# Kernel optimization log

Hardware: AMD Instinct MI355X
Metric: run time of the kernel (lower is better)

Reference implementation:

```python
import jax, jax.numpy as jnp
import numpy as np

NU, NI, NA, D = 100000, 100000, 10000, 64
N0 = NU + NI        # user+item graph nodes
N1 = NU + NA        # user+author graph nodes
E0, E1, E3, E4, E5 = 6_400_000, 3_520_000, 1_000_000, 1_000_000, 2_000_000
N_LAYERS = 3
EPS = 1e-12


def setup_inputs() -> dict:
    key = jax.random.key(0)
    ks = jax.random.split(key, 18)
    inp = {
        'emb_user': 0.1 * jax.random.normal(ks[0], (NU, D), jnp.float32),
        'emb_item': 0.1 * jax.random.normal(ks[1], (NI, D), jnp.float32),
        'emb_author': 0.1 * jax.random.normal(ks[2], (NA, D), jnp.float32),
        'g0_row': jax.random.randint(ks[3], (E0,), 0, N0, jnp.int32),
        'g0_col': jax.random.randint(ks[4], (E0,), 0, N0, jnp.int32),
        'g0_val': jax.random.uniform(ks[5], (E0,), jnp.float32) / 32.0,
        'g1_row': jax.random.randint(ks[6], (E1,), 0, N1, jnp.int32),
        'g1_col': jax.random.randint(ks[7], (E1,), 0, N1, jnp.int32),
        'g1_val': jax.random.uniform(ks[8], (E1,), jnp.float32) / 32.0,
        'g3_row': jax.random.randint(ks[9], (E3,), 0, NA, jnp.int32),
        'g3_col': jax.random.randint(ks[10], (E3,), 0, NI, jnp.int32),
        'g3_val': jax.random.uniform(ks[11], (E3,), jnp.float32),
        'g4_row': jax.random.randint(ks[12], (E4,), 0, NI, jnp.int32),
        'g4_col': jax.random.randint(ks[13], (E4,), 0, NA, jnp.int32),
        'g4_val': jax.random.uniform(ks[14], (E4,), jnp.float32),
        'g5_row': jax.random.randint(ks[15], (E5,), 0, NI, jnp.int32),
        'g5_col': jax.random.randint(ks[16], (E5,), 0, NI, jnp.int32),
        'g5_val': jax.random.uniform(ks[17], (E5,), jnp.float32),
    }
    return inp


def _spmm(row, col, val, x, n):
    # sparse [n, m] @ dense [m, d] via gather + segment_sum
    return jax.ops.segment_sum(val[:, None] * x[col], row, num_segments=n)


def _normalize(x):
    # F.normalize(x, p=2, dim=1)
    return x / jnp.maximum(jnp.linalg.norm(x, axis=1, keepdims=True), EPS)


def _one_propagate(row, col, val, a, b, n):
    # LightGCN propagation: stack per-layer features, mean across layers
    feats = jnp.concatenate([a, b], axis=0)  # [n, D]
    acc = feats
    cur = feats
    for _ in range(N_LAYERS):
        cur = _spmm(row, col, val, cur, n)
        acc = acc + cur
    out = acc / (N_LAYERS + 1)
    return out[: a.shape[0]], out[a.shape[0]:]


def reference(emb_user, emb_item, emb_author,
              g0_row, g0_col, g0_val,
              g1_row, g1_col, g1_val,
              g3_row, g3_col, g3_val,
              g4_row, g4_col, g4_val,
              g5_row, g5_col, g5_val):
    # atom branch: user-item graph
    atom_users, atom_items0 = _one_propagate(g0_row, g0_col, g0_val, emb_user, emb_item, N0)
    atom_authors = _normalize(_spmm(g3_row, g3_col, g3_val, atom_items0, NA))
    atom_items = 0.5 * _normalize(_spmm(g5_row, g5_col, g5_val, atom_items0, NI)) + 0.5 * atom_items0
    # non-atom branch: user-author graph
    non_atom_users, non_atom_authors = _one_propagate(g1_row, g1_col, g1_val, emb_user, emb_author, N1)
    non_atom_items = _normalize(_spmm(g4_row, g4_col, g4_val, non_atom_authors, NI))
    # computer() returns ([u0,u1],[i0,i1],[a0,a1]); concat to one array for a single baseline output
    return jnp.concatenate([atom_users, non_atom_users,
                            atom_items, non_atom_items,
                            atom_authors, non_atom_authors], axis=0)
```

## Files before the change

### kernel.cpp

```cpp
#include <hip/hip_runtime.h>

#define NUu 100000
#define NIi 100000
#define NAa 10000
#define DD  64
#define NN0 (NUu + NIi)
#define NN1 (NUu + NAa)

typedef unsigned int uint;
typedef unsigned short ushort;


__device__ __forceinline__ uint pack_bf2(float x, float y) {
    uint a = __float_as_uint(x);
    uint b = __float_as_uint(y);
    a = (a + 0x7fffu + ((a >> 16) & 1u)) >> 16;
    b = (b + 0x7fffu + ((b >> 16) & 1u)) & 0xffff0000u;
    return (a & 0xffffu) | b;
}
__device__ __forceinline__ float bflo(uint w) { return __uint_as_float(w << 16); }
__device__ __forceinline__ float bfhi(uint w) { return __uint_as_float(w & 0xffff0000u); }

__device__ __forceinline__ uint enc14(float v) {
    uint u = __float_as_uint(v);
    uint bf = (u + 0x7fffu + ((u >> 16) & 1u)) >> 16;
    return ((bf + 1u) >> 1) & 0x3FFFu;
}
__device__ __forceinline__ float dec14(uint e) { return __uint_as_float(e << 17); }

__global__ void k_f2bf3(const float4* __restrict__ su, const float4* __restrict__ si,
                        const float4* __restrict__ sa,
                        uint2* __restrict__ du, uint2* __restrict__ di,
                        uint2* __restrict__ da) {
    int i = blockIdx.x * blockDim.x + threadIdx.x;
    const int nu = NUu * 16, ni = NIi * 16, na = NAa * 16;
    const float4* s;
    uint2* d;
    int j;
    if (i < nu) { s = su; d = du; j = i; }
    else if (i < nu + ni) { s = si; d = di; j = i - nu; }
    else if (i < nu + ni + na) { s = sa; d = da; j = i - nu - ni; }
    else return;
    float4 v = s[j];
    uint2 o;
    o.x = pack_bf2(v.x, v.y);
    o.y = pack_bf2(v.z, v.w);
    d[j] = o;
}


#define P1_ITER 8
#define SEG_CAP 21760

__global__ void k_arenainit(int* __restrict__ bc,
                            int nb0, int nb1, int nb2, int nb3, int nb4,
                            int c0, int c1, int c2, int c3, int c4) {
    int t = threadIdx.x;
    if (t < nb0) bc[t] = t * c0;
    if (t < nb1) bc[512 + t] = t * c1;
    if (t < nb2) bc[1024 + t] = t * c2;
    if (t < nb3) bc[1536 + t] = t * c3;
    if (t < nb4) bc[2048 + t] = t * c4;
}

__global__ void __launch_bounds__(1024)
k_part1(const int* __restrict__ row, const int* __restrict__ col,
        const float* __restrict__ val, int* __restrict__ binCur,
        uint* __restrict__ stageC, ushort* __restrict__ stageR,
        int E, int shift, int nbins, int cap) {
    __shared__ int h[512];
    for (int t = threadIdx.x; t < nbins; t += blockDim.x) h[t] = 0;
    __syncthreads();
    int e0 = blockIdx.x * (blockDim.x * P1_ITER) + threadIdx.x;
    int r[P1_ITER];
#pragma unroll
    for (int i = 0; i < P1_ITER; ++i) {
        int e = e0 + i * blockDim.x;
        r[i] = (e < E) ? row[e] : -1;
        if (r[i] >= 0) atomicAdd(&h[r[i] >> shift], 1);
    }
    __syncthreads();
    for (int t = threadIdx.x; t < nbins; t += blockDim.x) {
        int c = h[t];
        h[t] = c ? atomicAdd(binCur + t, c) : 0;
    }
    __syncthreads();
#pragma unroll
    for (int i = 0; i < P1_ITER; ++i) {
        int e = e0 + i * blockDim.x;
        if (e < E) {
            int rr = r[i];
            int b = rr >> shift;
            int pos = atomicAdd(&h[b], 1);
            if (pos < (b + 1) * cap) {
                stageC[pos] = (((uint)col[e]) << 14) | enc14(val[e]);
                stageR[pos] = (ushort)(rr & ((1 << shift) - 1));
            }
        }
    }
}

__global__ void __launch_bounds__(1024)
k_part2(const int* __restrict__ binCur, const uint* __restrict__ stageC,
        const ushort* __restrict__ stageR, uint* __restrict__ csr,
        int2* __restrict__ rp2, int N, int shift, int cap) {
    __shared__ uint segc[SEG_CAP];
    __shared__ ushort segr[SEG_CAP];
    __shared__ int h[512];
    __shared__ int s[512];
    int tid = threadIdx.x;
    int rbase = blockIdx.x << shift;
    int nr = min(1 << shift, N - rbase);
    int es = blockIdx.x * cap;
    int ee = min(binCur[blockIdx.x], es + cap);
    int n = ee - es;
    if (tid < 512) h[tid] = 0;
    for (int i = tid; i < n; i += blockDim.x) {
        segc[i] = stageC[es + i];
        segr[i] = stageR[es + i];
    }
    __syncthreads();
    for (int i = tid; i < n; i += blockDim.x)
        atomicAdd(&h[segr[i]], 1);
    __syncthreads();
    int v = (tid < 512) ? h[tid] : 0;
    if (tid < 512) s[tid] = v;
    __syncthreads();
    for (int off = 1; off < 512; off <<= 1) {
        int t = (tid < 512 && tid >= off) ? s[tid - off] : 0;
        __syncthreads();
        if (tid < 512) s[tid] += t;
        __syncthreads();
    }
    if (tid < 512) h[tid] = es + s[tid] - v;
    if (tid < nr) {
        int st = es + s[tid] - v;
        rp2[rbase + tid] = make_int2(st, st + v);
    }
    __syncthreads();
    for (int i = tid; i < n; i += blockDim.x) {
        int pos = atomicAdd(&h[segr[i]], 1);
        csr[pos] = segc[i];
    }
}


template <bool SS>
__device__ __forceinline__ const uint* gb(uint pe, const uint* xbA, const uint* xbB,
                                          int split) {
    int c = (int)(pe >> 14);
    if (SS) return (c < split) ? xbA + (((long long)c) << 5)
                               : xbB + (((long long)(c - split)) << 5);
    return xbA + (((long long)c) << 5);
}

template <int MODE, bool SS>
__global__ void k_spmm(const int2* __restrict__ rp2, const uint* __restrict__ csr,
                       const uint* __restrict__ xbA, const uint* __restrict__ xbB, int split,
                       const float* __restrict__ embA, const float* __restrict__ embB,
                       const uint* __restrict__ y1b, const uint* __restrict__ y2b,
                       float* __restrict__ outU, float* __restrict__ outI,
                       uint* __restrict__ outIb,
                       uint* __restrict__ ob, float* __restrict__ yf,
                       const float* __restrict__ base, int nrows) {
    int r = blockIdx.x * (blockDim.x >> 6) + (threadIdx.x >> 6);
    if (r >= nrows) return;
    int lane = threadIdx.x & 63;
    int q = lane >> 4;
    int d8 = lane & 15;

    int2 se = rp2[r];
    int s0 = se.x, e0 = se.y;
    float a0 = 0.f, a1 = 0.f, a2 = 0.f, a3 = 0.f;
    int i = s0;
    for (; i + 32 <= e0; i += 32) {
        uint pe[8];
#pragma unroll
        for (int s = 0; s < 8; ++s)
            pe[s] = csr[i + 4 * s + q];
        uint2 wv[8];
#pragma unroll
        for (int s = 0; s < 8; ++s)
            wv[s] = *(const uint2*)(gb<SS>(pe[s], xbA, xbB, split) + 2 * d8);
#pragma unroll
        for (int s = 0; s < 8; ++s) {
            float v = dec14(pe[s] & 0x3FFFu);
            a0 += v * bflo(wv[s].x); a1 += v * bfhi(wv[s].x);
            a2 += v * bflo(wv[s].y); a3 += v * bfhi(wv[s].y);
        }
    }
    for (; i + 8 <= e0; i += 8) {
        uint p0 = csr[i + q];
        uint p1 = csr[i + 4 + q];
        uint2 w0 = *(const uint2*)(gb<SS>(p0, xbA, xbB, split) + 2 * d8);
        uint2 w1 = *(const uint2*)(gb<SS>(p1, xbA, xbB, split) + 2 * d8);
        float v0 = dec14(p0 & 0x3FFFu);
        float v1 = dec14(p1 & 0x3FFFu);
        a0 += v0 * bflo(w0.x); a1 += v0 * bfhi(w0.x);
        a2 += v0 * bflo(w0.y); a3 += v0 * bfhi(w0.y);
        a0 += v1 * bflo(w1.x); a1 += v1 * bfhi(w1.x);
        a2 += v1 * bflo(w1.y); a3 += v1 * bfhi(w1.y);
    }
    for (; i < e0; i += 4) {
        int idx = i + q;
        uint pe = (idx < e0) ? csr[idx] : 0u;
        uint2 wv = *(const uint2*)(gb<SS>(pe, xbA, xbB, split) + 2 * d8);
        float v = dec14(pe & 0x3FFFu);
        a0 += v * bflo(wv.x); a1 += v * bfhi(wv.x); a2 += v * bflo(wv.y); a3 += v * bfhi(wv.y);
    }
    a0 += __shfl_xor(a0, 16); a0 += __shfl_xor(a0, 32);
    a1 += __shfl_xor(a1, 16); a1 += __shfl_xor(a1, 32);
    a2 += __shfl_xor(a2, 16); a2 += __shfl_xor(a2, 32);
    a3 += __shfl_xor(a3, 16); a3 += __shfl_xor(a3, 32);

    long long off4 = (((long long)r) << 6) + 4 * d8;
    long long offw = (((long long)r) << 5) + 2 * d8;

    if (MODE == 0) {
        if (q == 0) {
            uint2 o;
            o.x = pack_bf2(a0, a1);
            o.y = pack_bf2(a2, a3);
            *(uint2*)(ob + offw) = o;
        }
    } else if (MODE == 1) {
        if (q == 0) {
            float4 e4;
            if (r < split) e4 = *(const float4*)(embA + off4);
            else           e4 = *(const float4*)(embB + (off4 - (((long long)split) << 6)));
            uint2 w1 = *(const uint2*)(y1b + offw);
            uint2 w2 = *(const uint2*)(y2b + offw);
            float s0f = 0.25f * (e4.x + bflo(w1.x) + bflo(w2.x) + a0);
            float s1f = 0.25f * (e4.y + bfhi(w1.x) + bfhi(w2.x) + a1);
            float s2f = 0.25f * (e4.z + bflo(w1.y) + bflo(w2.y) + a2);
            float s3f = 0.25f * (e4.w + bfhi(w1.y) + bfhi(w2.y) + a3);
            float4 o;
            o.x = s0f; o.y = s1f; o.z = s2f; o.w = s3f;
            if (r < split) {
                *(float4*)(outU + off4) = o;
            } else {
                *(float4*)(outI + (off4 - (((long long)split) << 6))) = o;
                if (outIb) {
                    uint2 ob2;
                    ob2.x = pack_bf2(s0f, s1f);
                    ob2.y = pack_bf2(s2f, s3f);
                    *(uint2*)(outIb + (((long long)(r - split)) << 5) + 2 * d8) = ob2;
                }
            }
        }
    } else {
        float sq = a0 * a0 + a1 * a1 + a2 * a2 + a3 * a3;
        sq += __shfl_xor(sq, 1); sq += __shfl_xor(sq, 2);
        sq += __shfl_xor(sq, 4); sq += __shfl_xor(sq, 8);
        float inv = 1.0f / fmaxf(sqrtf(sq), 1e-12f);
        if (q == 0) {
            float4 o;
            if (MODE == 2) {
                o.x = a0 * inv; o.y = a1 * inv; o.z = a2 * inv; o.w = a3 * inv;
            } else {
                float4 b4 = *(const float4*)(base + off4);
                o.x = 0.5f * a0 * inv + 0.5f * b4.x;
                o.y = 0.5f * a1 * inv + 0.5f * b4.y;
                o.z = 0.5f * a2 * inv + 0.5f * b4.z;
                o.w = 0.5f * a3 * inv + 0.5f * b4.w;
            }
            *(float4*)(yf + off4) = o;
        }
    }
}


static inline int nblk(long long n, int b) { return (int)((n + b - 1) / b); }
static inline size_t al256(size_t x) { return (x + 255) & ~(size_t)255; }
#define AMAX 8450000

extern "C" void kernel_launch(void* const* d_in, const int* in_sizes, int n_in,
                              void* d_out, int out_size, void* d_ws, size_t ws_size,
                              hipStream_t stream) {
    const float* emb_user   = (const float*)d_in[0];
    const float* emb_item   = (const float*)d_in[1];
    const float* emb_author = (const float*)d_in[2];
    const int*   g0r = (const int*)d_in[3];
    const int*   g0c = (const int*)d_in[4];
    const float* g0v = (const float*)d_in[5];
    const int*   g1r = (const int*)d_in[6];
    const int*   g1c = (const int*)d_in[7];
    const float* g1v = (const float*)d_in[8];
    const int*   g3r = (const int*)d_in[9];
    const int*   g3c = (const int*)d_in[10];
    const float* g3v = (const float*)d_in[11];
    const int*   g4r = (const int*)d_in[12];
    const int*   g4c = (const int*)d_in[13];
    const float* g4v = (const float*)d_in[14];
    const int*   g5r = (const int*)d_in[15];
    const int*   g5c = (const int*)d_in[16];
    const float* g5v = (const float*)d_in[17];

    const int E0 = in_sizes[3];
    const int E1 = in_sizes[6];
    const int E3 = in_sizes[9];
    const int E4 = in_sizes[12];
    const int E5 = in_sizes[15];

    float* out = (float*)d_out;

    char* w = (char*)d_ws;
    int2* rp2     = (int2*)w; w += al256((size_t)(NN0 + 1) * 8);
    int*  binCur5 = (int*)w;  w += al256((size_t)5 * 512 * 4);
    uint* csr     = (uint*)w; w += al256((size_t)AMAX * 4);
    uint* embUb   = (uint*)w; w += al256((size_t)NUu * 32 * 4);
    uint* embIb   = (uint*)w; w += al256((size_t)NIi * 32 * 4);
    uint* embAb   = (uint*)w; w += al256((size_t)NAa * 32 * 4);
    uint* y1b     = (uint*)w; w += al256((size_t)NN0 * 32 * 4);
    uint* y2b     = (uint*)w; w += al256((size_t)NN0 * 32 * 4);
    float* items0  = (float*)w; w += al256((size_t)NIi * DD * 4);
    uint*  items0b = (uint*)w;  w += al256((size_t)NIi * 32 * 4);
    uint*  oAuthNb = (uint*)w;  w += al256((size_t)NAa * 32 * 4);
    uint*   stageC = (uint*)y1b;
    ushort* stageR = (ushort*)((char*)y1b + al256((size_t)AMAX * 4));

    const int B = 256;

    struct G { int nbins, shift, cap; };
    auto geo = [](int E, int N, int shift) {
        G g;
        g.shift = shift;
        g.nbins = (N + (1 << shift) - 1) >> shift;
        int cap = E / g.nbins + E / (4 * g.nbins) + 1024;
        g.cap = cap > SEG_CAP ? SEG_CAP : cap;
        return g;
    };
    G gg0 = geo(E0, NN0, 9), gg1 = geo(E1, NN1, 9), gg3 = geo(E3, NAa, 5),
      gg5 = geo(E5, NIi, 8), gg4 = geo(E4, NIi, 8);

    float* oUserA = out;
    float* oUserN = out + (long long)NUu * DD;
    float* oItemA = out + (long long)200000 * DD;
    float* oItemN = out + (long long)300000 * DD;
    float* oAuthA = out + (long long)400000 * DD;
    float* oAuthN = out + (long long)410000 * DD;

    k_f2bf3<<<nblk((long long)(NUu + NIi + NAa) * 16, B), B, 0, stream>>>(
        (const float4*)emb_user, (const float4*)emb_item, (const float4*)emb_author,
        (uint2*)embUb, (uint2*)embIb, (uint2*)embAb);
    k_arenainit<<<1, 512, 0, stream>>>(binCur5,
        gg0.nbins, gg1.nbins, gg3.nbins, gg5.nbins, gg4.nbins,
        gg0.cap, gg1.cap, gg3.cap, gg5.cap, gg4.cap);

    auto build = [&](const int* row, const int* col, const float* val,
                     int E, int N, const G& g, int slot) {
        int* bc = binCur5 + slot * 512;
        k_part1<<<nblk(E, 1024 * P1_ITER), 1024, 0, stream>>>(row, col, val, bc,
                                                              stageC, stageR,
                                                              E, g.shift, g.nbins, g.cap);
        k_part2<<<g.nbins, 1024, 0, stream>>>(bc, stageC, stageR, csr, rp2,
                                              N, g.shift, g.cap);
    };

    build(g0r, g0c, g0v, E0, NN0, gg0, 0);
    k_spmm<0, true><<<nblk(NN0, 4), B, 0, stream>>>(rp2, csr, embUb, embIb, NUu,
                                                    nullptr, nullptr, nullptr, nullptr,
                                                    nullptr, nullptr, nullptr,
                                                    y1b, nullptr, nullptr, NN0);
    k_spmm<0, false><<<nblk(NN0, 4), B, 0, stream>>>(rp2, csr, y1b, nullptr, 0,
                                                     nullptr, nullptr, nullptr, nullptr,
                                                     nullptr, nullptr, nullptr,
                                                     y2b, nullptr, nullptr, NN0);
    k_spmm<1, false><<<nblk(NN0, 4), B, 0, stream>>>(rp2, csr, y2b, nullptr, NUu,
                                                     emb_user, emb_item, y1b, y2b,
                                                     oUserA, items0, items0b,
                                                     nullptr, nullptr, nullptr, NN0);

    build(g1r, g1c, g1v, E1, NN1, gg1, 1);
    k_spmm<0, true><<<nblk(NN1, 4), B, 0, stream>>>(rp2, csr, embUb, embAb, NUu,
                                                    nullptr, nullptr, nullptr, nullptr,
                                                    nullptr, nullptr, nullptr,
                                                    y1b, nullptr, nullptr, NN1);
    k_spmm<0, false><<<nblk(NN1, 4), B, 0, stream>>>(rp2, csr, y1b, nullptr, 0,
                                                     nullptr, nullptr, nullptr, nullptr,
                                                     nullptr, nullptr, nullptr,
                                                     y2b, nullptr, nullptr, NN1);
    k_spmm<1, false><<<nblk(NN1, 4), B, 0, stream>>>(rp2, csr, y2b, nullptr, NUu,
                                                     emb_user, emb_author, y1b, y2b,
                                                     oUserN, oAuthN, oAuthNb,
                                                     nullptr, nullptr, nullptr, NN1);

    build(g3r, g3c, g3v, E3, NAa, gg3, 2);
    k_spmm<2, false><<<nblk(NAa, 4), B, 0, stream>>>(rp2, csr, items0b, nullptr, 0,
                                                     nullptr, nullptr, nullptr, nullptr,
                                                     nullptr, nullptr, nullptr,
                                                     nullptr, oAuthA, nullptr, NAa);

    build(g5r, g5c, g5v, E5, NIi, gg5, 3);
    k_spmm<3, false><<<nblk(NIi, 4), B, 0, stream>>>(rp2, csr, items0b, nullptr, 0,
                                                     nullptr, nullptr, nullptr, nullptr,
                                                     nullptr, nullptr, nullptr,
                                                     nullptr, oItemA, items0, NIi);

    build(g4r, g4c, g4v, E4, NIi, gg4, 4);
    k_spmm<2, false><<<nblk(NIi, 4), B, 0, stream>>>(rp2, csr, oAuthNb, nullptr, 0,
                                                     nullptr, nullptr, nullptr, nullptr,
                                                     nullptr, nullptr, nullptr,
                                                     nullptr, oItemN, nullptr, NIi);
}
```

Baseline: 1.219 ms.

## Pack staging entries as int2 and use smaller CSR build bins

Staging for the CSR build now stores one int2 per edge (local row and column packed in x, raw float value in y) instead of separate uint and ushort arrays. The 14-bit value encoding moves from partition pass 1 into pass 2. Graphs g0 and g1 now use 256-row bins instead of 512, so there are more bins and blocks in pass 2, each with a smaller shared segment and less shared-memory pressure (LDS). Bin capacity slack is tightened, and the histogram and arena arrays are widened to 1024 bins. The tighter caps raise the risk of overflowing a bin and silently dropping edges.

```diff
diff --git a/kernel.cpp b/kernel.cpp
--- a/kernel.cpp
+++ b/kernel.cpp
@@ -50,25 +50,24 @@
 
 
 #define P1_ITER 8
-#define SEG_CAP 21760
+#define SEG_CAP 9472
 
 __global__ void k_arenainit(int* __restrict__ bc,
                             int nb0, int nb1, int nb2, int nb3, int nb4,
                             int c0, int c1, int c2, int c3, int c4) {
     int t = threadIdx.x;
     if (t < nb0) bc[t] = t * c0;
-    if (t < nb1) bc[512 + t] = t * c1;
-    if (t < nb2) bc[1024 + t] = t * c2;
-    if (t < nb3) bc[1536 + t] = t * c3;
-    if (t < nb4) bc[2048 + t] = t * c4;
+    if (t < nb1) bc[1024 + t] = t * c1;
+    if (t < nb2) bc[2048 + t] = t * c2;
+    if (t < nb3) bc[3072 + t] = t * c3;
+    if (t < nb4) bc[4096 + t] = t * c4;
 }
 
 __global__ void __launch_bounds__(1024)
 k_part1(const int* __restrict__ row, const int* __restrict__ col,
         const float* __restrict__ val, int* __restrict__ binCur,
-        uint* __restrict__ stageC, ushort* __restrict__ stageR,
-        int E, int shift, int nbins, int cap) {
-    __shared__ int h[512];
+        int2* __restrict__ stage, int E, int shift, int nbins, int cap) {
+    __shared__ int h[1024];
     for (int t = threadIdx.x; t < nbins; t += blockDim.x) h[t] = 0;
     __syncthreads();
     int e0 = blockIdx.x * (blockDim.x * P1_ITER) + threadIdx.x;
@@ -93,19 +92,19 @@
             int b = rr >> shift;
             int pos = atomicAdd(&h[b], 1);
             if (pos < (b + 1) * cap) {
-                stageC[pos] = (((uint)col[e]) << 14) | enc14(val[e]);
-                stageR[pos] = (ushort)(rr & ((1 << shift) - 1));
+                int2 p;
+                p.x = ((rr & ((1 << shift) - 1)) << 18) | col[e];
+                p.y = __float_as_int(val[e]);
+                stage[pos] = p;
             }
         }
     }
 }
 
 __global__ void __launch_bounds__(1024)
-k_part2(const int* __restrict__ binCur, const uint* __restrict__ stageC,
-        const ushort* __restrict__ stageR, uint* __restrict__ csr,
-        int2* __restrict__ rp2, int N, int shift, int cap) {
-    __shared__ uint segc[SEG_CAP];
-    __shared__ ushort segr[SEG_CAP];
+k_part2(const int* __restrict__ binCur, const int2* __restrict__ stage,
+        uint* __restrict__ csr, int2* __restrict__ rp2, int N, int shift, int cap) {
+    __shared__ int2 seg[SEG_CAP];
     __shared__ int h[512];
     __shared__ int s[512];
     int tid = threadIdx.x;
@@ -115,13 +114,10 @@
     int ee = min(binCur[blockIdx.x], es + cap);
     int n = ee - es;
     if (tid < 512) h[tid] = 0;
-    for (int i = tid; i < n; i += blockDim.x) {
-        segc[i] = stageC[es + i];
-        segr[i] = stageR[es + i];
-    }
+    for (int i = tid; i < n; i += blockDim.x) seg[i] = stage[es + i];
     __syncthreads();
     for (int i = tid; i < n; i += blockDim.x)
-        atomicAdd(&h[segr[i]], 1);
+        atomicAdd(&h[seg[i].x >> 18], 1);
     __syncthreads();
     int v = (tid < 512) ? h[tid] : 0;
     if (tid < 512) s[tid] = v;
@@ -139,8 +135,9 @@
     }
     __syncthreads();
     for (int i = tid; i < n; i += blockDim.x) {
-        int pos = atomicAdd(&h[segr[i]], 1);
-        csr[pos] = segc[i];
+        int2 p = seg[i];
+        int pos = atomicAdd(&h[p.x >> 18], 1);
+        csr[pos] = (((uint)(p.x & 0x3ffff)) << 14) | enc14(__int_as_float(p.y));
     }
 }
 
@@ -272,7 +269,7 @@
 
 static inline int nblk(long long n, int b) { return (int)((n + b - 1) / b); }
 static inline size_t al256(size_t x) { return (x + 255) & ~(size_t)255; }
-#define AMAX 8450000
+#define AMAX 7250000
 
 extern "C" void kernel_launch(void* const* d_in, const int* in_sizes, int n_in,
                               void* d_out, int out_size, void* d_ws, size_t ws_size,
@@ -306,18 +303,17 @@
 
     char* w = (char*)d_ws;
     int2* rp2     = (int2*)w; w += al256((size_t)(NN0 + 1) * 8);
-    int*  binCur5 = (int*)w;  w += al256((size_t)5 * 512 * 4);
+    int*  binCur5 = (int*)w;  w += al256((size_t)5 * 1024 * 4);
     uint* csr     = (uint*)w; w += al256((size_t)AMAX * 4);
     uint* embUb   = (uint*)w; w += al256((size_t)NUu * 32 * 4);
     uint* embIb   = (uint*)w; w += al256((size_t)NIi * 32 * 4);
     uint* embAb   = (uint*)w; w += al256((size_t)NAa * 32 * 4);
     uint* y1b     = (uint*)w; w += al256((size_t)NN0 * 32 * 4);
     uint* y2b     = (uint*)w; w += al256((size_t)NN0 * 32 * 4);
-    float* items0  = (float*)w; w += al256((size_t)NIi * DD * 4);
-    uint*  items0b = (uint*)w;  w += al256((size_t)NIi * 32 * 4);
-    uint*  oAuthNb = (uint*)w;  w += al256((size_t)NAa * 32 * 4);
-    uint*   stageC = (uint*)y1b;
-    ushort* stageR = (ushort*)((char*)y1b + al256((size_t)AMAX * 4));
+    uint* items0b = (uint*)w; w += al256((size_t)NIi * 32 * 4);
+    float* items0 = (float*)w; w += al256((size_t)NIi * DD * 4);
+    uint* oAuthNb = (uint*)w; w += al256((size_t)NAa * 32 * 4);
+    int2* stage = (int2*)y1b;
 
     const int B = 256;
 
@@ -326,11 +322,11 @@
         G g;
         g.shift = shift;
         g.nbins = (N + (1 << shift) - 1) >> shift;
-        int cap = E / g.nbins + E / (4 * g.nbins) + 1024;
+        int cap = E / g.nbins + E / (16 * g.nbins) + 512;
         g.cap = cap > SEG_CAP ? SEG_CAP : cap;
         return g;
     };
-    G gg0 = geo(E0, NN0, 9), gg1 = geo(E1, NN1, 9), gg3 = geo(E3, NAa, 5),
+    G gg0 = geo(E0, NN0, 8), gg1 = geo(E1, NN1, 8), gg3 = geo(E3, NAa, 5),
       gg5 = geo(E5, NIi, 8), gg4 = geo(E4, NIi, 8);
 
     float* oUserA = out;
@@ -343,18 +339,17 @@
     k_f2bf3<<<nblk((long long)(NUu + NIi + NAa) * 16, B), B, 0, stream>>>(
         (const float4*)emb_user, (const float4*)emb_item, (const float4*)emb_author,
         (uint2*)embUb, (uint2*)embIb, (uint2*)embAb);
-    k_arenainit<<<1, 512, 0, stream>>>(binCur5,
+    k_arenainit<<<1, 1024, 0, stream>>>(binCur5,
         gg0.nbins, gg1.nbins, gg3.nbins, gg5.nbins, gg4.nbins,
         gg0.cap, gg1.cap, gg3.cap, gg5.cap, gg4.cap);
 
     auto build = [&](const int* row, const int* col, const float* val,
                      int E, int N, const G& g, int slot) {
-        int* bc = binCur5 + slot * 512;
+        int* bc = binCur5 + slot * 1024;
         k_part1<<<nblk(E, 1024 * P1_ITER), 1024, 0, stream>>>(row, col, val, bc,
-                                                              stageC, stageR,
-                                                              E, g.shift, g.nbins, g.cap);
-        k_part2<<<g.nbins, 1024, 0, stream>>>(bc, stageC, stageR, csr, rp2,
-                                              N, g.shift, g.cap);
+                                                              stage, E, g.shift,
+                                                              g.nbins, g.cap);
+        k_part2<<<g.nbins, 1024, 0, stream>>>(bc, stage, csr, rp2, N, g.shift, g.cap);
     };
 
     build(g0r, g0c, g0v, E0, NN0, gg0, 0);
```

New measurement: 1.076 ms, median of 2. 11.7% less time.
